# Kernel optimization log

Hardware: AMD Instinct MI355X
Metric: run time of the kernel (lower is better)

The kernel has to match this reference:

```python
import jax, jax.numpy as jnp
import numpy as np

# ---- Build Cayley tables for projective GA G(3,0,1), basis ordered by grade ----
_BLADES = [(), (0,), (1,), (2,), (3,), (0,1), (0,2), (0,3), (1,2), (1,3), (2,3),
           (0,1,2), (0,1,3), (0,2,3), (1,2,3), (0,1,2,3)]
_IDX = {b: i for i, b in enumerate(_BLADES)}

def _blade_mul(a, b, metric):
    """Multiply basis blades a*b. Returns (sign, result_blade); sign=0 if it vanishes."""
    arr = list(a) + list(b)
    sign = 1
    changed = True
    while changed:
        changed = False
        for i in range(len(arr) - 1):
            if arr[i] > arr[i + 1]:
                arr[i], arr[i + 1] = arr[i + 1], arr[i]
                sign = -sign
                changed = True
            elif arr[i] == arr[i + 1]:
                sign *= metric[arr[i]]
                del arr[i:i + 2]
                changed = True
                break
    return sign, tuple(arr)

def _build_tables():
    metric = [0, 1, 1, 1]  # e0^2 = 0 (degenerate), e1^2=e2^2=e3^2=1
    G = np.zeros((16, 16, 16), np.float32)  # geometric product
    W = np.zeros((16, 16, 16), np.float32)  # outer (wedge) product
    for a in _BLADES:
        for b in _BLADES:
            s, r = _blade_mul(a, b, metric)
            if s != 0:
                G[_IDX[a], _IDX[b], _IDX[r]] = s
            if not (set(a) & set(b)):
                s2, r2 = _blade_mul(a, b, [1, 1, 1, 1])
                W[_IDX[a], _IDX[b], _IDX[r2]] = s2
    # Right-complement dual: dual(e_a) = s * e_c with e_a ^ dual(e_a) = e0123
    full = (0, 1, 2, 3)
    dual_idx = np.zeros(16, np.int32)
    dual_sign = np.zeros(16, np.float32)
    for a in _BLADES:
        c = tuple(sorted(set(full) - set(a)))
        s, _ = _blade_mul(a, c, [1, 1, 1, 1])
        dual_idx[_IDX[a]] = _IDX[c]
        dual_sign[_IDX[a]] = s
    # Coefficient map: dual(x)[j] = dual_sign[dual_idx[j]] * x[dual_idx[j]]
    out_sign = dual_sign[dual_idx]
    return jnp.asarray(G), jnp.asarray(W), jnp.asarray(dual_idx), jnp.asarray(out_sign)

_G, _W, _DUAL_IDX, _DUAL_SIGN = _build_tables()
_PSS = 15  # index of pseudoscalar e0123

def _dual(x):
    return x[..., _DUAL_IDX] * _DUAL_SIGN


def setup_inputs() -> dict:
    key = jax.random.key(0)
    k1, k2, k3 = jax.random.split(key, 3)
    B, T, C = 64, 8192, 16
    return {
        "x": jax.random.normal(k1, (B, T, C), dtype=jnp.float32),
        "y": jax.random.normal(k2, (B, T, C), dtype=jnp.float32),
        "ref": jax.random.normal(k3, (B, T, C), dtype=jnp.float32),
    }


def reference(x, y, ref):
    # Geometric product over the Cayley table
    gp = jnp.einsum("bti,btj,ijk->btk", x, y, _G)
    # E(3)-equivariant join: ref_e0123 * dual(dual(x) ^ dual(y))
    wedge = jnp.einsum("bti,btj,ijk->btk", _dual(x), _dual(y), _W)
    join = ref[..., _PSS:_PSS + 1] * _dual(wedge)
    return jnp.concatenate([gp, join], axis=-1)  # (B, T, 32)
```

## Files before the change

kernel.cpp:

```cpp
#include <hip/hip_runtime.h>

namespace ga {

constexpr int MASK[16]        = {0,1,2,4,8,3,5,9,6,10,12,7,11,13,14,15};
constexpr int IDX_OF_MASK[16] = {0,1,2,5,3,6,8,11,4,7,9,12,10,13,14,15};

constexpr int popc(int v) { int c = 0; while (v) { c += v & 1; v >>= 1; } return c; }

constexpr int reorder_sign(int a, int b) {
    int s = 0; int t = a >> 1;
    while (t) { s += popc(t & b); t >>= 1; }
    return (s & 1) ? -1 : 1;
}

struct Term { signed char i, j, k, s; };

struct GPTab { Term t[192]; };
constexpr GPTab build_gp() {
    GPTab T{}; int n = 0;
    for (int i = 0; i < 16; i++)
        for (int j = 0; j < 16; j++) {
            int a = MASK[i], b = MASK[j];
            if (a & b & 1) continue;
            T.t[n].i = (signed char)i;
            T.t[n].j = (signed char)j;
            T.t[n].k = (signed char)IDX_OF_MASK[a ^ b];
            T.t[n].s = (signed char)reorder_sign(a, b);
            n++;
        }
    return T;
}

struct JNTab { Term t[81]; };
constexpr JNTab build_join() {
    JNTab T{}; int n = 0;
    int didx[16] = {}, dsgn[16] = {};
    for (int i = 0; i < 16; i++) {
        int a = MASK[i], c = (~a) & 0xF;
        didx[i] = IDX_OF_MASK[c];
        dsgn[i] = reorder_sign(a, c);
    }
    for (int i = 0; i < 16; i++)
        for (int j = 0; j < 16; j++) {
            int p = didx[i], q = didx[j];
            int a = MASK[p], b = MASK[q];
            if (a & b) continue;
            int m = IDX_OF_MASK[a | b];
            int k = didx[m];
            int s = dsgn[i] * dsgn[j] * dsgn[m] * reorder_sign(a, b);
            T.t[n].i = (signed char)i;
            T.t[n].j = (signed char)j;
            T.t[n].k = (signed char)k;
            T.t[n].s = (signed char)s;
            n++;
        }
    return T;
}

constexpr GPTab G = build_gp();
constexpr JNTab J = build_join();

}

constexpr int BUF_FLOATS = 2304;
constexpr int OSTRIDE    = 36;

typedef const __attribute__((address_space(1))) void* gas_ptr;
typedef __attribute__((address_space(3))) void*       las_ptr;

__global__ __launch_bounds__(64, 2)
void MVGeometricBilinear_kernel(const float* __restrict__ x,
                                const float* __restrict__ y,
                                const float* __restrict__ ref,
                                float* __restrict__ out,
                                int nchunks, int niter)
{
    __shared__ __align__(16) float buf[2][BUF_FLOATS];
    __shared__ __align__(16) float rbuf[2][64];

    const int lane = threadIdx.x;
    long chunk = (long)blockIdx.x * niter;
    long cend  = chunk + niter;
    if (cend > nchunks) cend = nchunks;
    if (chunk >= cend) return;

    auto dma_chunk = [&](long c, int b) {
        const float4* gx = reinterpret_cast<const float4*>(x) + c * 256;
        const float4* gy = reinterpret_cast<const float4*>(y) + c * 256;
#pragma unroll
        for (int k = 0; k < 4; k++) {
            __builtin_amdgcn_global_load_lds((gas_ptr)(gx + k * 64 + lane),
                                             (las_ptr)(&buf[b][k * 256]), 16, 0, 0);
            __builtin_amdgcn_global_load_lds((gas_ptr)(gy + k * 64 + lane),
                                             (las_ptr)(&buf[b][1024 + k * 256]), 16, 0, 0);
        }
        __builtin_amdgcn_global_load_lds((gas_ptr)(ref + (c * 64 + lane) * 16 + 15),
                                         (las_ptr)(&rbuf[b][0]), 4, 0, 0);
    };

    int cur = 0;
    dma_chunk(chunk, 0);

    while (true) {
        const long next = chunk + 1;
        const bool pf = (next < cend);

        if (pf) {
            dma_chunk(next, cur ^ 1);
            asm volatile("s_waitcnt vmcnt(9)" ::: "memory");
        } else {
            asm volatile("s_waitcnt vmcnt(0)" ::: "memory");
        }

        const float* bx = &buf[cur][0];
        const float* by = &buf[cur][1024];
        float xx[16], yy[16];
#pragma unroll
        for (int k = 0; k < 4; k++) {
            const float4 vx = *reinterpret_cast<const float4*>(bx + lane * 16 + k * 4);
            const float4 vy = *reinterpret_cast<const float4*>(by + lane * 16 + k * 4);
            xx[4*k+0] = vx.x; xx[4*k+1] = vx.y; xx[4*k+2] = vx.z; xx[4*k+3] = vx.w;
            yy[4*k+0] = vy.x; yy[4*k+1] = vy.y; yy[4*k+2] = vy.z; yy[4*k+3] = vy.w;
        }
        const float r = rbuf[cur][lane];

        float gp[16] = {0.f, 0.f, 0.f, 0.f, 0.f, 0.f, 0.f, 0.f,
                        0.f, 0.f, 0.f, 0.f, 0.f, 0.f, 0.f, 0.f};
        float jn[16] = {0.f, 0.f, 0.f, 0.f, 0.f, 0.f, 0.f, 0.f,
                        0.f, 0.f, 0.f, 0.f, 0.f, 0.f, 0.f, 0.f};
#pragma unroll
        for (int t = 0; t < 192; t++) {
            const int ti = ga::G.t[t].i, tj = ga::G.t[t].j, tk = ga::G.t[t].k;
            const float v = xx[ti] * yy[tj];
            if (ga::G.t[t].s > 0) gp[tk] += v; else gp[tk] -= v;
        }
#pragma unroll
        for (int t = 0; t < 81; t++) {
            const int ti = ga::J.t[t].i, tj = ga::J.t[t].j, tk = ga::J.t[t].k;
            const float v = xx[ti] * yy[tj];
            if (ga::J.t[t].s > 0) jn[tk] += v; else jn[tk] -= v;
        }

        asm volatile("" ::: "memory");

        float* lo = &buf[cur][0];
#pragma unroll
        for (int k = 0; k < 4; k++)
            *reinterpret_cast<float4*>(lo + lane * OSTRIDE + k * 4) =
                make_float4(gp[4*k+0], gp[4*k+1], gp[4*k+2], gp[4*k+3]);
#pragma unroll
        for (int k = 0; k < 4; k++)
            *reinterpret_cast<float4*>(lo + lane * OSTRIDE + 16 + k * 4) =
                make_float4(r * jn[4*k+0], r * jn[4*k+1], r * jn[4*k+2], r * jn[4*k+3]);

        float4* go = reinterpret_cast<float4*>(out) + chunk * 512;
#pragma unroll
        for (int c = 0; c < 8; c++) {
            const int g  = lane + 64 * c;
            const int p  = g >> 3;
            const int ch = g & 7;
            go[g] = *reinterpret_cast<const float4*>(lo + p * OSTRIDE + ch * 4);
        }

        asm volatile("" ::: "memory");

        if (!pf) break;
        cur ^= 1;
        chunk = next;
    }
}

__global__ __launch_bounds__(64)
void MVGeometricBilinear_tail(const float* __restrict__ x,
                              const float* __restrict__ y,
                              const float* __restrict__ ref,
                              float* __restrict__ out,
                              int start, int npts)
{
    int pt = start + blockIdx.x * 64 + threadIdx.x;
    if (pt >= npts) return;
    float xx[16], yy[16];
#pragma unroll
    for (int k = 0; k < 16; k++) { xx[k] = x[(size_t)pt*16+k]; yy[k] = y[(size_t)pt*16+k]; }
    const float r = ref[(size_t)pt*16+15];
    float gp[16] = {}, jn[16] = {};
#pragma unroll
    for (int t = 0; t < 192; t++) {
        const float v = xx[ga::G.t[t].i] * yy[ga::G.t[t].j];
        if (ga::G.t[t].s > 0) gp[ga::G.t[t].k] += v; else gp[ga::G.t[t].k] -= v;
    }
#pragma unroll
    for (int t = 0; t < 81; t++) {
        const float v = xx[ga::J.t[t].i] * yy[ga::J.t[t].j];
        if (ga::J.t[t].s > 0) jn[ga::J.t[t].k] += v; else jn[ga::J.t[t].k] -= v;
    }
#pragma unroll
    for (int k = 0; k < 16; k++) out[(size_t)pt*32+k] = gp[k];
#pragma unroll
    for (int k = 0; k < 16; k++) out[(size_t)pt*32+16+k] = r * jn[k];
}

extern "C" void kernel_launch(void* const* d_in, const int* in_sizes, int n_in,
                              void* d_out, int out_size, void* d_ws, size_t ws_size,
                              hipStream_t stream) {
    const float* x   = (const float*)d_in[0];
    const float* y   = (const float*)d_in[1];
    const float* ref = (const float*)d_in[2];
    float* out = (float*)d_out;

    const int npts    = in_sizes[0] / 16;
    const int nchunks = npts / 64;
    const int niter   = 4;
    const int blocks  = (nchunks + niter - 1) / niter;

    if (nchunks > 0) {
        MVGeometricBilinear_kernel<<<blocks, 64, 0, stream>>>(
            x, y, ref, out, nchunks, niter);
    }

    const int rem = npts - nchunks * 64;
    if (rem > 0) {
        MVGeometricBilinear_tail<<<(rem + 63) / 64, 64, 0, stream>>>(
            x, y, ref, out, nchunks * 64, npts);
    }
}
```

Baseline: 146.6 us.

## Replace per-block double-buffered chunk loop with one chunk per block

Removes the software double-buffering loop, so each 64-thread block now loads, computes and writes exactly one 64-point chunk. The LDS footprint is halved and the launch-bounds occupancy hint rises from 2 to 4, which lets more blocks sit resident and hide latency through parallelism instead of explicit prefetch. The cost is that loads inside a block no longer overlap compute, and there are four times as many blocks to launch.

```diff
diff --git a/kernel.cpp b/kernel.cpp
--- a/kernel.cpp
+++ b/kernel.cpp
@@ -68,105 +68,84 @@
 typedef const __attribute__((address_space(1))) void* gas_ptr;
 typedef __attribute__((address_space(3))) void*       las_ptr;
 
-__global__ __launch_bounds__(64, 2)
+__global__ __launch_bounds__(64, 4)
 void MVGeometricBilinear_kernel(const float* __restrict__ x,
                                 const float* __restrict__ y,
                                 const float* __restrict__ ref,
                                 float* __restrict__ out,
-                                int nchunks, int niter)
+                                int nchunks)
 {
-    __shared__ __align__(16) float buf[2][BUF_FLOATS];
-    __shared__ __align__(16) float rbuf[2][64];
+    __shared__ __align__(16) float buf[BUF_FLOATS];
+    __shared__ __align__(16) float rbuf[64];
 
     const int lane = threadIdx.x;
-    long chunk = (long)blockIdx.x * niter;
-    long cend  = chunk + niter;
-    if (cend > nchunks) cend = nchunks;
-    if (chunk >= cend) return;
-
-    auto dma_chunk = [&](long c, int b) {
-        const float4* gx = reinterpret_cast<const float4*>(x) + c * 256;
-        const float4* gy = reinterpret_cast<const float4*>(y) + c * 256;
+    const long chunk = blockIdx.x;
+    if (chunk >= nchunks) return;
+
+    {
+        const float4* gx = reinterpret_cast<const float4*>(x) + chunk * 256;
+        const float4* gy = reinterpret_cast<const float4*>(y) + chunk * 256;
 #pragma unroll
         for (int k = 0; k < 4; k++) {
             __builtin_amdgcn_global_load_lds((gas_ptr)(gx + k * 64 + lane),
-                                             (las_ptr)(&buf[b][k * 256]), 16, 0, 0);
+                                             (las_ptr)(&buf[k * 256]), 16, 0, 0);
             __builtin_amdgcn_global_load_lds((gas_ptr)(gy + k * 64 + lane),
-                                             (las_ptr)(&buf[b][1024 + k * 256]), 16, 0, 0);
+                                             (las_ptr)(&buf[1024 + k * 256]), 16, 0, 0);
         }
-        __builtin_amdgcn_global_load_lds((gas_ptr)(ref + (c * 64 + lane) * 16 + 15),
-                                         (las_ptr)(&rbuf[b][0]), 4, 0, 0);
-    };
-
-    int cur = 0;
-    dma_chunk(chunk, 0);
-
-    while (true) {
-        const long next = chunk + 1;
-        const bool pf = (next < cend);
-
-        if (pf) {
-            dma_chunk(next, cur ^ 1);
-            asm volatile("s_waitcnt vmcnt(9)" ::: "memory");
-        } else {
-            asm volatile("s_waitcnt vmcnt(0)" ::: "memory");
-        }
-
-        const float* bx = &buf[cur][0];
-        const float* by = &buf[cur][1024];
-        float xx[16], yy[16];
-#pragma unroll
-        for (int k = 0; k < 4; k++) {
-            const float4 vx = *reinterpret_cast<const float4*>(bx + lane * 16 + k * 4);
-            const float4 vy = *reinterpret_cast<const float4*>(by + lane * 16 + k * 4);
-            xx[4*k+0] = vx.x; xx[4*k+1] = vx.y; xx[4*k+2] = vx.z; xx[4*k+3] = vx.w;
-            yy[4*k+0] = vy.x; yy[4*k+1] = vy.y; yy[4*k+2] = vy.z; yy[4*k+3] = vy.w;
-        }
-        const float r = rbuf[cur][lane];
-
-        float gp[16] = {0.f, 0.f, 0.f, 0.f, 0.f, 0.f, 0.f, 0.f,
-                        0.f, 0.f, 0.f, 0.f, 0.f, 0.f, 0.f, 0.f};
-        float jn[16] = {0.f, 0.f, 0.f, 0.f, 0.f, 0.f, 0.f, 0.f,
-                        0.f, 0.f, 0.f, 0.f, 0.f, 0.f, 0.f, 0.f};
-#pragma unroll
-        for (int t = 0; t < 192; t++) {
-            const int ti = ga::G.t[t].i, tj = ga::G.t[t].j, tk = ga::G.t[t].k;
-            const float v = xx[ti] * yy[tj];
-            if (ga::G.t[t].s > 0) gp[tk] += v; else gp[tk] -= v;
-        }
-#pragma unroll
-        for (int t = 0; t < 81; t++) {
-            const int ti = ga::J.t[t].i, tj = ga::J.t[t].j, tk = ga::J.t[t].k;
-            const float v = xx[ti] * yy[tj];
-            if (ga::J.t[t].s > 0) jn[tk] += v; else jn[tk] -= v;
-        }
-
-        asm volatile("" ::: "memory");
-
-        float* lo = &buf[cur][0];
-#pragma unroll
-        for (int k = 0; k < 4; k++)
-            *reinterpret_cast<float4*>(lo + lane * OSTRIDE + k * 4) =
-                make_float4(gp[4*k+0], gp[4*k+1], gp[4*k+2], gp[4*k+3]);
-#pragma unroll
-        for (int k = 0; k < 4; k++)
-            *reinterpret_cast<float4*>(lo + lane * OSTRIDE + 16 + k * 4) =
-                make_float4(r * jn[4*k+0], r * jn[4*k+1], r * jn[4*k+2], r * jn[4*k+3]);
-
-        float4* go = reinterpret_cast<float4*>(out) + chunk * 512;
-#pragma unroll
-        for (int c = 0; c < 8; c++) {
-            const int g  = lane + 64 * c;
-            const int p  = g >> 3;
-            const int ch = g & 7;
-            go[g] = *reinterpret_cast<const float4*>(lo + p * OSTRIDE + ch * 4);
-        }
-
-        asm volatile("" ::: "memory");
-
-        if (!pf) break;
-        cur ^= 1;
-        chunk = next;
+        __builtin_amdgcn_global_load_lds((gas_ptr)(ref + (chunk * 64 + lane) * 16 + 15),
+                                         (las_ptr)(&rbuf[0]), 4, 0, 0);
+    }
+
+    asm volatile("s_waitcnt vmcnt(0)" ::: "memory");
+
+    const float* bx = &buf[0];
+    const float* by = &buf[1024];
+    float xx[16], yy[16];
+#pragma unroll
+    for (int k = 0; k < 4; k++) {
+        const float4 vx = *reinterpret_cast<const float4*>(bx + lane * 16 + k * 4);
+        const float4 vy = *reinterpret_cast<const float4*>(by + lane * 16 + k * 4);
+        xx[4*k+0] = vx.x; xx[4*k+1] = vx.y; xx[4*k+2] = vx.z; xx[4*k+3] = vx.w;
+        yy[4*k+0] = vy.x; yy[4*k+1] = vy.y; yy[4*k+2] = vy.z; yy[4*k+3] = vy.w;
+    }
+    const float r = rbuf[lane];
+
+    float gp[16] = {0.f, 0.f, 0.f, 0.f, 0.f, 0.f, 0.f, 0.f,
+                    0.f, 0.f, 0.f, 0.f, 0.f, 0.f, 0.f, 0.f};
+    float jn[16] = {0.f, 0.f, 0.f, 0.f, 0.f, 0.f, 0.f, 0.f,
+                    0.f, 0.f, 0.f, 0.f, 0.f, 0.f, 0.f, 0.f};
+#pragma unroll
+    for (int t = 0; t < 192; t++) {
+        const int ti = ga::G.t[t].i, tj = ga::G.t[t].j, tk = ga::G.t[t].k;
+        const float v = xx[ti] * yy[tj];
+        if (ga::G.t[t].s > 0) gp[tk] += v; else gp[tk] -= v;
+    }
+#pragma unroll
+    for (int t = 0; t < 81; t++) {
+        const int ti = ga::J.t[t].i, tj = ga::J.t[t].j, tk = ga::J.t[t].k;
+        const float v = xx[ti] * yy[tj];
+        if (ga::J.t[t].s > 0) jn[tk] += v; else jn[tk] -= v;
+    }
+
+    asm volatile("" ::: "memory");
+
+    float* lo = &buf[0];
+#pragma unroll
+    for (int k = 0; k < 4; k++)
+        *reinterpret_cast<float4*>(lo + lane * OSTRIDE + k * 4) =
+            make_float4(gp[4*k+0], gp[4*k+1], gp[4*k+2], gp[4*k+3]);
+#pragma unroll
+    for (int k = 0; k < 4; k++)
+        *reinterpret_cast<float4*>(lo + lane * OSTRIDE + 16 + k * 4) =
+            make_float4(r * jn[4*k+0], r * jn[4*k+1], r * jn[4*k+2], r * jn[4*k+3]);
+
+    float4* go = reinterpret_cast<float4*>(out) + chunk * 512;
+#pragma unroll
+    for (int c = 0; c < 8; c++) {
+        const int g  = lane + 64 * c;
+        const int p  = g >> 3;
+        const int ch = g & 7;
+        go[g] = *reinterpret_cast<const float4*>(lo + p * OSTRIDE + ch * 4);
     }
 }
 
@@ -210,12 +189,10 @@
 
     const int npts    = in_sizes[0] / 16;
     const int nchunks = npts / 64;
-    const int niter   = 4;
-    const int blocks  = (nchunks + niter - 1) / niter;
 
     if (nchunks > 0) {
-        MVGeometricBilinear_kernel<<<blocks, 64, 0, stream>>>(
-            x, y, ref, out, nchunks, niter);
+        MVGeometricBilinear_kernel<<<nchunks, 64, 0, stream>>>(
+            x, y, ref, out, nchunks);
     }
 
     const int rem = npts - nchunks * 64;
```

Result: no change. 144.8 us (-1.3%).
